# Performance work log

Hardware: AMD Instinct MI355X
Metric: run time of the kernel (lower is better)

The kernel has to match this reference:

```python
import jax, jax.numpy as jnp
import numpy as np

B, T, D, H = 4, 4096, 2048, 128  # batch, seq, n_embd, head_size


def setup_inputs() -> dict:
    key = jax.random.key(0)
    ks = jax.random.split(key, 7)
    s = 1.0 / np.sqrt(D)
    return {
        "x": jax.random.normal(ks[0], (B, T, D), dtype=jnp.float32),
        "Wk": jax.random.normal(ks[1], (D, H), dtype=jnp.float32) * s,
        "bk": jax.random.normal(ks[2], (H,), dtype=jnp.float32) * 0.02,
        "Wq": jax.random.normal(ks[3], (D, H), dtype=jnp.float32) * s,
        "bq": jax.random.normal(ks[4], (H,), dtype=jnp.float32) * 0.02,
        "Wv": jax.random.normal(ks[5], (D, H), dtype=jnp.float32) * s,
        "bv": jax.random.normal(ks[6], (H,), dtype=jnp.float32) * 0.02,
    }


def reference(x, Wk, bk, Wq, bq, Wv, bv):
    # q, k, v projections: [B, T, H]
    q = x @ Wq + bq
    k = x @ Wk + bk
    v = x @ Wv + bv
    scale = jnp.asarray(H, x.dtype) ** -0.5
    # causal attention scores [B, T, T]
    scores = jnp.einsum("bth,bsh->bts", q, k) * scale
    causal = jnp.tril(jnp.ones((T, T), dtype=bool))
    scores = jnp.where(causal, scores, jnp.asarray(-jnp.inf, x.dtype))
    probs = jax.nn.softmax(scores, axis=-1)
    # output [B, T, H]
    return jnp.einsum("bts,bsh->bth", probs, v)
```

## Files before the change

### kernel.cpp

```cpp
#include <hip/hip_runtime.h>

namespace {

typedef float f32x4 __attribute__((ext_vector_type(4)));
typedef short bf16x8 __attribute__((ext_vector_type(8)));

constexpr float SM_SCALE = 0.08838834764831845f;

#define MFMA16(a, b, c) __builtin_amdgcn_mfma_f32_16x16x32_bf16((a), (b), (c), 0, 0, 0)

__device__ __forceinline__ unsigned short bf16_rne(float x) {
  unsigned u = __float_as_uint(x);
  u += 0x7fffu + ((u >> 16) & 1u);
  return (unsigned short)(u >> 16);
}
__device__ __forceinline__ float bf16f(unsigned short h) {
  return __uint_as_float(((unsigned)h) << 16);
}
__device__ __forceinline__ void gld16(const void* g, void* l) {
  __builtin_amdgcn_global_load_lds(
      (const __attribute__((address_space(1))) unsigned int*)g,
      (__attribute__((address_space(3))) unsigned int*)l, 16, 0, 0);
}
__device__ __forceinline__ uint4 pack8(const unsigned short* h) {
  uint4 u;
  u.x = (unsigned)h[0] | ((unsigned)h[1] << 16);
  u.y = (unsigned)h[2] | ((unsigned)h[3] << 16);
  u.z = (unsigned)h[4] | ((unsigned)h[5] << 16);
  u.w = (unsigned)h[6] | ((unsigned)h[7] << 16);
  return u;
}

__global__ void prep_w(const float* __restrict__ Wq, const float* __restrict__ Wk,
                       const float* __restrict__ Wv,
                       unsigned short* __restrict__ WtH, unsigned short* __restrict__ WtL) {
  const int tg = blockIdx.x * 256 + threadIdx.x;
  const int mi = tg >> 15;
  const int rem = tg & 32767;
  const int n = rem & 127;
  const int k0 = (rem >> 7) * 8;
  const float* W = (mi == 0) ? Wq : ((mi == 1) ? Wk : Wv);
  unsigned short hv[8], lv[8];
#pragma unroll
  for (int e = 0; e < 8; ++e) {
    float xx = W[(size_t)(k0 + e) * 128 + n];
    unsigned short hh = bf16_rne(xx);
    hv[e] = hh;
    lv[e] = bf16_rne(xx - bf16f(hh));
  }
  const size_t off = (size_t)mi * 262144 + (size_t)n * 2048 + k0;
  *(uint4*)(WtH + off) = pack8(hv);
  *(uint4*)(WtL + off) = pack8(lv);
}

__global__ __launch_bounds__(256, 2) void qkv_gemm(
    const float* __restrict__ x,
    const unsigned short* __restrict__ WtH, const unsigned short* __restrict__ WtL,
    const float* __restrict__ bq, const float* __restrict__ bk, const float* __restrict__ bv,
    unsigned short* __restrict__ qh, unsigned short* __restrict__ ql,
    unsigned short* __restrict__ kh, unsigned short* __restrict__ kl,
    unsigned short* __restrict__ vTh, unsigned short* __restrict__ vTl) {
  __shared__ __align__(16) unsigned short sm[32768];
  unsigned short* AsH = sm;
  unsigned short* AsL = sm + 8192;
  unsigned short* BsH = sm + 16384;
  unsigned short* BsL = sm + 24576;

  const int mi = blockIdx.x;
  const int m0 = blockIdx.y * 128;
  const int t = threadIdx.x;
  const int w = t >> 6, l = t & 63, g = l >> 4, lm = l & 15;
  const int wr = w >> 1, wc = w & 1;
  const int sw = (lm & 7) << 3;
  const unsigned short* WhP = WtH + (size_t)mi * 262144;
  const unsigned short* WlP = WtL + (size_t)mi * 262144;
  const float* bias = (mi == 0) ? bq : ((mi == 1) ? bk : bv);

  const int arow = t >> 4, ac4 = (t & 15) * 4;
  const int nsub = l >> 3, kk0 = (l & 7) * 8;

  const f32x4 zf = {0.f, 0.f, 0.f, 0.f};
  f32x4 acc[4][4];
#pragma unroll
  for (int m = 0; m < 4; ++m)
#pragma unroll
    for (int n = 0; n < 4; ++n) acc[m][n] = zf;

  float4 av[8];
#pragma unroll
  for (int i = 0; i < 8; ++i)
    av[i] = *(const float4*)(x + (size_t)(m0 + i * 16 + arow) * 2048 + ac4);

  for (int kc = 0; kc < 2048; kc += 64) {
    __syncthreads();
#pragma unroll
    for (int i = 0; i < 4; ++i) {
      const int blk = w * 4 + i;
      const int n = blk * 8 + nsub;
      const size_t go = (size_t)n * 2048 + kc + (kk0 ^ ((n & 7) << 3));
      gld16(WhP + go, BsH + blk * 512);
      gld16(WlP + go, BsL + blk * 512);
    }
#pragma unroll
    for (int i = 0; i < 8; ++i) {
      const int row = i * 16 + arow;
      const int idx = row * 64 + (ac4 ^ ((row & 7) << 3));
      ushort4 hh, ll;
      hh.x = bf16_rne(av[i].x); ll.x = bf16_rne(av[i].x - bf16f(hh.x));
      hh.y = bf16_rne(av[i].y); ll.y = bf16_rne(av[i].y - bf16f(hh.y));
      hh.z = bf16_rne(av[i].z); ll.z = bf16_rne(av[i].z - bf16f(hh.z));
      hh.w = bf16_rne(av[i].w); ll.w = bf16_rne(av[i].w - bf16f(hh.w));
      *(ushort4*)&AsH[idx] = hh;
      *(ushort4*)&AsL[idx] = ll;
    }
    __syncthreads();

    if (kc + 64 < 2048) {
#pragma unroll
      for (int i = 0; i < 8; ++i)
        av[i] = *(const float4*)(x + (size_t)(m0 + i * 16 + arow) * 2048 + kc + 64 + ac4);
    }

    __builtin_amdgcn_s_setprio(1);
#pragma unroll
    for (int ks = 0; ks < 2; ++ks) {
      const int kb = ks * 32 + g * 8;
      bf16x8 ah[4], al_[4], bh_[4], bl_[4];
#pragma unroll
      for (int m = 0; m < 4; ++m) {
        const int row = wr * 64 + m * 16 + lm;
        const int idx = row * 64 + (kb ^ sw);
        ah[m] = *(const bf16x8*)&AsH[idx];
        al_[m] = *(const bf16x8*)&AsL[idx];
      }
#pragma unroll
      for (int n = 0; n < 4; ++n) {
        const int row = wc * 64 + n * 16 + lm;
        const int idx = row * 64 + (kb ^ sw);
        bh_[n] = *(const bf16x8*)&BsH[idx];
        bl_[n] = *(const bf16x8*)&BsL[idx];
      }
#pragma unroll
      for (int m = 0; m < 4; ++m)
#pragma unroll
        for (int n = 0; n < 4; ++n) {
          acc[m][n] = MFMA16(ah[m], bh_[n], acc[m][n]);
          acc[m][n] = MFMA16(ah[m], bl_[n], acc[m][n]);
          acc[m][n] = MFMA16(al_[m], bh_[n], acc[m][n]);
        }
    }
    __builtin_amdgcn_s_setprio(0);
  }

  __syncthreads();
  float* Cb = (float*)sm;
#pragma unroll
  for (int n = 0; n < 4; ++n) {
    const int col = wc * 64 + n * 16 + lm;
    const float bn = bias[col];
#pragma unroll
    for (int m = 0; m < 4; ++m)
#pragma unroll
      for (int r = 0; r < 4; ++r)
        Cb[(wr * 64 + m * 16 + g * 4 + r) * 128 + col] = acc[m][n][r] + bn;
  }
  __syncthreads();

  if (mi < 2) {
    unsigned short* oh = (mi == 0) ? qh : kh;
    unsigned short* ol = (mi == 0) ? ql : kl;
    const int c8 = (t & 15) * 8;
#pragma unroll
    for (int i = 0; i < 8; ++i) {
      const int row = i * 16 + (t >> 4);
      float v8[8];
      *(float4*)(v8)     = *(const float4*)&Cb[row * 128 + c8];
      *(float4*)(v8 + 4) = *(const float4*)&Cb[row * 128 + c8 + 4];
      unsigned short h8[8], l8[8];
#pragma unroll
      for (int j = 0; j < 8; ++j) {
        h8[j] = bf16_rne(v8[j]);
        l8[j] = bf16_rne(v8[j] - bf16f(h8[j]));
      }
      const size_t o = (size_t)(m0 + row) * 128 + c8;
      *(uint4*)(oh + o) = pack8(h8);
      *(uint4*)(ol + o) = pack8(l8);
    }
  } else {
    const int bidx = m0 >> 12, tb0 = m0 & 4095;
    const int tb8 = (t & 15) * 8;
#pragma unroll
    for (int i = 0; i < 8; ++i) {
      const int h = i * 16 + (t >> 4);
      float v8[8];
#pragma unroll
      for (int j = 0; j < 8; ++j) v8[j] = Cb[(tb8 + j) * 128 + h];
      unsigned short h8[8], l8[8];
#pragma unroll
      for (int j = 0; j < 8; ++j) {
        h8[j] = bf16_rne(v8[j]);
        l8[j] = bf16_rne(v8[j] - bf16f(h8[j]));
      }
      const size_t o = ((size_t)bidx * 128 + h) * 4096 + tb0 + tb8;
      *(uint4*)(vTh + o) = pack8(h8);
      *(uint4*)(vTl + o) = pack8(l8);
    }
  }
}

__global__ __launch_bounds__(256, 2) void attn(
    const unsigned short* __restrict__ qh, const unsigned short* __restrict__ ql,
    const unsigned short* __restrict__ kh, const unsigned short* __restrict__ kl,
    const unsigned short* __restrict__ vTh, const unsigned short* __restrict__ vTl,
    float* __restrict__ OP, float* __restrict__ ML) {
  __shared__ __align__(16) unsigned short sm[40960];
  unsigned short* KhL = sm;
  unsigned short* KlL = sm + 8192;
  unsigned short* VhL = sm + 16384;
  unsigned short* VlL = sm + 24576;
  unsigned short* PhL = sm + 32768;
  unsigned short* PlL = sm + 36864;

  const int b = blockIdx.y, bx = blockIdx.x;
  const int pj = bx >> 2, s = bx & 3;
  const int t = threadIdx.x, w = t >> 6, l = t & 63, g = l >> 4, lm = l & 15;
  const int sw8 = (lm & 7) << 3;
  const size_t bT = (size_t)b * 4096;
  const f32x4 zf = {0.f, 0.f, 0.f, 0.f};

  const int krow_l = l >> 4;
  const int kh8 = (l & 15) * 8;
  const int vrow_l = l >> 3;
  const int vk8 = (l & 7) * 8;

  for (int pass = 0; pass < 2; ++pass) {
    const int qb = pass ? (63 - pj) : pj;
    const int q0 = qb * 64;
    const int part = b * 256 + qb * 4 + s;

    bf16x8 qfh[4], qfl[4];
    const size_t qoff = (bT + q0 + w * 16 + lm) * 128;
#pragma unroll
    for (int ks = 0; ks < 4; ++ks) {
      qfh[ks] = *(const bf16x8*)(qh + qoff + ks * 32 + g * 8);
      qfl[ks] = *(const bf16x8*)(ql + qoff + ks * 32 + g * 8);
    }

    f32x4 o[8];
#pragma unroll
    for (int n = 0; n < 8; ++n) o[n] = zf;
    float mrow = -1e30f, lrow = 0.f;
    const int qg = q0 + w * 16 + lm;
    const int nt = qb + 1;

    for (int ti = s; ti < nt; ti += 4) {
      const int t0 = ti * 64;
      __syncthreads();
#pragma unroll
      for (int i = 0; i < 4; ++i) {
        const int j = w * 4 + i;
        const int krow = 4 * j + krow_l;
        const size_t kgo = (bT + t0 + krow) * 128 + (kh8 ^ ((krow & 7) << 3));
        gld16(kh + kgo, KhL + j * 512);
        gld16(kl + kgo, KlL + j * 512);
        const int hrow = 8 * j + vrow_l;
        const size_t vgo = ((size_t)b * 128 + hrow) * 4096 + t0 + (vk8 ^ ((hrow & 7) << 3));
        gld16(vTh + vgo, VhL + j * 512);
        gld16(vTl + vgo, VlL + j * 512);
      }
      __syncthreads();

      f32x4 sa[4] = {zf, zf, zf, zf};
      __builtin_amdgcn_s_setprio(1);
#pragma unroll
      for (int ks = 0; ks < 4; ++ks) {
        const int kb = (ks * 32 + g * 8) ^ sw8;
#pragma unroll
        for (int m = 0; m < 4; ++m) {
          const bf16x8 kf = *(const bf16x8*)&KhL[(m * 16 + lm) * 128 + kb];
          const bf16x8 lf = *(const bf16x8*)&KlL[(m * 16 + lm) * 128 + kb];
          sa[m] = MFMA16(kf, qfh[ks], sa[m]);
          sa[m] = MFMA16(kf, qfl[ks], sa[m]);
          sa[m] = MFMA16(lf, qfh[ks], sa[m]);
        }
      }
      __builtin_amdgcn_s_setprio(0);

      float pv_[16];
      float mt = -1e30f;
#pragma unroll
      for (int m = 0; m < 4; ++m)
#pragma unroll
        for (int r = 0; r < 4; ++r) {
          const int kvg = t0 + m * 16 + g * 4 + r;
          const float sv = (kvg <= qg) ? sa[m][r] * SM_SCALE : -1e30f;
          pv_[m * 4 + r] = sv;
          mt = fmaxf(mt, sv);
        }
      mt = fmaxf(mt, __shfl_xor(mt, 16));
      mt = fmaxf(mt, __shfl_xor(mt, 32));
      const float mnew = fmaxf(mrow, mt);
      const float sc = __expf(mrow - mnew);
      float lsum = 0.f;
#pragma unroll
      for (int j = 0; j < 16; ++j) {
        const float pe = (pv_[j] > -9e29f) ? __expf(pv_[j] - mnew) : 0.f;
        pv_[j] = pe;
        lsum += pe;
      }
      lsum += __shfl_xor(lsum, 16);
      lsum += __shfl_xor(lsum, 32);
      lrow = lrow * sc + lsum;
      mrow = mnew;
      float scr[4];
#pragma unroll
      for (int r = 0; r < 4; ++r) scr[r] = __shfl(sc, g * 4 + r);
#pragma unroll
      for (int n = 0; n < 8; ++n)
#pragma unroll
        for (int r = 0; r < 4; ++r) o[n][r] *= scr[r];

      const int wb = w * 1024;
#pragma unroll
      for (int m = 0; m < 4; ++m)
#pragma unroll
        for (int j2 = 0; j2 < 2; ++j2) {
          const int kv0 = m * 16 + g * 4 + j2 * 2;
          const float p0f = pv_[m * 4 + j2 * 2];
          const float p1f = pv_[m * 4 + j2 * 2 + 1];
          ushort2 h2, l2;
          h2.x = bf16_rne(p0f); l2.x = bf16_rne(p0f - bf16f(h2.x));
          h2.y = bf16_rne(p1f); l2.y = bf16_rne(p1f - bf16f(h2.y));
          *(ushort2*)&PhL[wb + lm * 64 + (kv0 ^ sw8)] = h2;
          *(ushort2*)&PlL[wb + lm * 64 + (kv0 ^ sw8)] = l2;
        }
      const bf16x8 pAh0 = *(const bf16x8*)&PhL[wb + lm * 64 + ((g * 8) ^ sw8)];
      const bf16x8 pAl0 = *(const bf16x8*)&PlL[wb + lm * 64 + ((g * 8) ^ sw8)];
      const bf16x8 pAh1 = *(const bf16x8*)&PhL[wb + lm * 64 + ((32 + g * 8) ^ sw8)];
      const bf16x8 pAl1 = *(const bf16x8*)&PlL[wb + lm * 64 + ((32 + g * 8) ^ sw8)];

      __builtin_amdgcn_s_setprio(1);
#pragma unroll
      for (int n = 0; n < 8; ++n) {
        const int vb = (n * 16 + lm) * 64;
        const bf16x8 vh0 = *(const bf16x8*)&VhL[vb + ((g * 8) ^ sw8)];
        const bf16x8 vl0 = *(const bf16x8*)&VlL[vb + ((g * 8) ^ sw8)];
        o[n] = MFMA16(pAh0, vh0, o[n]);
        o[n] = MFMA16(pAh0, vl0, o[n]);
        o[n] = MFMA16(pAl0, vh0, o[n]);
        const bf16x8 vh1 = *(const bf16x8*)&VhL[vb + ((32 + g * 8) ^ sw8)];
        const bf16x8 vl1 = *(const bf16x8*)&VlL[vb + ((32 + g * 8) ^ sw8)];
        o[n] = MFMA16(pAh1, vh1, o[n]);
        o[n] = MFMA16(pAh1, vl1, o[n]);
        o[n] = MFMA16(pAl1, vh1, o[n]);
      }
      __builtin_amdgcn_s_setprio(0);
    }

    float* OPp = OP + (size_t)part * 8192;
#pragma unroll
    for (int n = 0; n < 8; ++n)
#pragma unroll
      for (int r = 0; r < 4; ++r)
        OPp[(size_t)(w * 16 + g * 4 + r) * 128 + n * 16 + lm] = o[n][r];
    if (l < 16) {
      ML[((size_t)part * 64 + w * 16 + l) * 2 + 0] = mrow;
      ML[((size_t)part * 64 + w * 16 + l) * 2 + 1] = lrow;
    }
  }
}

__global__ void combine(const float* __restrict__ OP, const float* __restrict__ ML,
                        float* __restrict__ out) {
  const int x = blockIdx.x;
  const int b = x >> 6, qb = x & 63;
  const int p0 = b * 256 + qb * 4;
  const int t = threadIdx.x;
  const int r = t >> 2, hq = (t & 3) * 32;
  float m[4], ll[4];
#pragma unroll
  for (int s2 = 0; s2 < 4; ++s2) {
    m[s2]  = ML[((size_t)(p0 + s2) * 64 + r) * 2 + 0];
    ll[s2] = ML[((size_t)(p0 + s2) * 64 + r) * 2 + 1];
  }
  const float mx = fmaxf(fmaxf(m[0], m[1]), fmaxf(m[2], m[3]));
  float wgt[4], den = 0.f;
#pragma unroll
  for (int s2 = 0; s2 < 4; ++s2) {
    wgt[s2] = __expf(m[s2] - mx);
    den += wgt[s2] * ll[s2];
  }
  const float inv = 1.f / den;
  float* op = out + ((size_t)(b * 4096 + qb * 64 + r)) * 128 + hq;
#pragma unroll
  for (int j = 0; j < 8; ++j) {
    float ax = 0.f, ay = 0.f, az = 0.f, aw = 0.f;
#pragma unroll
    for (int s2 = 0; s2 < 4; ++s2) {
      const float4 pv = *(const float4*)(OP + ((size_t)(p0 + s2) * 64 + r) * 128 + hq + j * 4);
      ax += wgt[s2] * pv.x; ay += wgt[s2] * pv.y;
      az += wgt[s2] * pv.z; aw += wgt[s2] * pv.w;
    }
    float4 ov; ov.x = ax * inv; ov.y = ay * inv; ov.z = az * inv; ov.w = aw * inv;
    *(float4*)(op + j * 4) = ov;
  }
}

}

extern "C" void kernel_launch(void* const* d_in, const int* in_sizes, int n_in,
                              void* d_out, int out_size, void* d_ws, size_t ws_size,
                              hipStream_t stream) {
  const float* x  = (const float*)d_in[0];
  const float* Wk = (const float*)d_in[1];
  const float* bk = (const float*)d_in[2];
  const float* Wq = (const float*)d_in[3];
  const float* bq = (const float*)d_in[4];
  const float* Wv = (const float*)d_in[5];
  const float* bv = (const float*)d_in[6];
  float* out = (float*)d_out;

  unsigned short* WtH = (unsigned short*)d_ws;
  unsigned short* WtL = WtH + 786432;
  unsigned short* qh  = WtL + 786432;
  unsigned short* ql  = qh + 2097152;
  unsigned short* kh  = ql + 2097152;
  unsigned short* kl  = kh + 2097152;
  unsigned short* vTh = kl + 2097152;
  unsigned short* vTl = vTh + 2097152;
  float* OP = (float*)(vTl + 2097152);
  float* ML = OP + (size_t)1024 * 8192;

  prep_w<<<384, 256, 0, stream>>>(Wq, Wk, Wv, WtH, WtL);
  qkv_gemm<<<dim3(3, 128), 256, 0, stream>>>(x, WtH, WtL, bq, bk, bv,
                                             qh, ql, kh, kl, vTh, vTl);
  attn<<<dim3(128, 4), 256, 0, stream>>>(qh, ql, kh, kl, vTh, vTl, OP, ML);
  combine<<<256, 256, 0, stream>>>(OP, ML, out);
}
```

Baseline: 380.7 us.

## Retile QKV GEMM with double-buffered weights and 128-row attention blocks

The QKV GEMM now uses 64-row M tiles over a 768-block remapped grid and double-buffers the weight tiles in LDS, so the next K-chunk's loads overlap the current MFMAs. The attention kernel now gives each block 128 query rows (two 16-row tiles per wave) instead of running two 64-row passes, so each K/V tile loaded into LDS is reused across twice as many queries. Partial buffers and the combine kernel are re-indexed to match. The cost is more registers per wave in attention (doubled accumulators and Q fragments), less even causal load balancing, and more LDS in the GEMM.

```diff
diff --git a/kernel.cpp b/kernel.cpp
--- a/kernel.cpp
+++ b/kernel.cpp
@@ -60,14 +60,14 @@
     unsigned short* __restrict__ qh, unsigned short* __restrict__ ql,
     unsigned short* __restrict__ kh, unsigned short* __restrict__ kl,
     unsigned short* __restrict__ vTh, unsigned short* __restrict__ vTl) {
-  __shared__ __align__(16) unsigned short sm[32768];
+  __shared__ __align__(16) unsigned short sm[40960];
   unsigned short* AsH = sm;
-  unsigned short* AsL = sm + 8192;
-  unsigned short* BsH = sm + 16384;
-  unsigned short* BsL = sm + 24576;
-
-  const int mi = blockIdx.x;
-  const int m0 = blockIdx.y * 128;
+  unsigned short* AsL = sm + 4096;
+
+  const int bid = blockIdx.x;
+  const int L = 96 * (bid & 7) + (bid >> 3);
+  const int mi = L % 3;
+  const int m0 = (L / 3) * 64;
   const int t = threadIdx.x;
   const int w = t >> 6, l = t & 63, g = l >> 4, lm = l & 15;
   const int wr = w >> 1, wc = w & 1;
@@ -77,33 +77,34 @@
   const float* bias = (mi == 0) ? bq : ((mi == 1) ? bk : bv);
 
   const int arow = t >> 4, ac4 = (t & 15) * 4;
-  const int nsub = l >> 3, kk0 = (l & 7) * 8;
+  const int brow_l = l >> 3, bk8 = (l & 7) * 8;
 
   const f32x4 zf = {0.f, 0.f, 0.f, 0.f};
-  f32x4 acc[4][4];
-#pragma unroll
-  for (int m = 0; m < 4; ++m)
+  f32x4 acc[2][4];
+#pragma unroll
+  for (int m = 0; m < 2; ++m)
 #pragma unroll
     for (int n = 0; n < 4; ++n) acc[m][n] = zf;
 
-  float4 av[8];
-#pragma unroll
-  for (int i = 0; i < 8; ++i)
-    av[i] = *(const float4*)(x + (size_t)(m0 + i * 16 + arow) * 2048 + ac4);
-
+  float4 av[4];
+#pragma unroll
+  for (int i = 0; i < 4; ++i) {
+    const int j = w * 4 + i;
+    const int n = j * 8 + brow_l;
+    const size_t go = (size_t)n * 2048 + 0 + (bk8 ^ ((n & 7) << 3));
+    gld16(WhP + go, sm + 8192 + j * 512);
+    gld16(WlP + go, sm + 16384 + j * 512);
+  }
+#pragma unroll
+  for (int i = 0; i < 4; ++i)
+    av[i] = *(const float4*)(x + (size_t)(m0 + arow + 16 * i) * 2048 + ac4);
+
+  int cur = 0;
   for (int kc = 0; kc < 2048; kc += 64) {
     __syncthreads();
 #pragma unroll
     for (int i = 0; i < 4; ++i) {
-      const int blk = w * 4 + i;
-      const int n = blk * 8 + nsub;
-      const size_t go = (size_t)n * 2048 + kc + (kk0 ^ ((n & 7) << 3));
-      gld16(WhP + go, BsH + blk * 512);
-      gld16(WlP + go, BsL + blk * 512);
-    }
-#pragma unroll
-    for (int i = 0; i < 8; ++i) {
-      const int row = i * 16 + arow;
+      const int row = arow + 16 * i;
       const int idx = row * 64 + (ac4 ^ ((row & 7) << 3));
       ushort4 hh, ll;
       hh.x = bf16_rne(av[i].x); ll.x = bf16_rne(av[i].x - bf16f(hh.x));
@@ -117,18 +118,28 @@
 
     if (kc + 64 < 2048) {
 #pragma unroll
-      for (int i = 0; i < 8; ++i)
-        av[i] = *(const float4*)(x + (size_t)(m0 + i * 16 + arow) * 2048 + kc + 64 + ac4);
-    }
-
+      for (int i = 0; i < 4; ++i) {
+        const int j = w * 4 + i;
+        const int n = j * 8 + brow_l;
+        const size_t go = (size_t)n * 2048 + (kc + 64) + (bk8 ^ ((n & 7) << 3));
+        gld16(WhP + go, sm + 8192 + (cur ^ 1) * 16384 + j * 512);
+        gld16(WlP + go, sm + 8192 + (cur ^ 1) * 16384 + 8192 + j * 512);
+      }
+#pragma unroll
+      for (int i = 0; i < 4; ++i)
+        av[i] = *(const float4*)(x + (size_t)(m0 + arow + 16 * i) * 2048 + kc + 64 + ac4);
+    }
+
+    const unsigned short* BH = sm + 8192 + cur * 16384;
+    const unsigned short* BL = BH + 8192;
     __builtin_amdgcn_s_setprio(1);
 #pragma unroll
     for (int ks = 0; ks < 2; ++ks) {
       const int kb = ks * 32 + g * 8;
-      bf16x8 ah[4], al_[4], bh_[4], bl_[4];
-#pragma unroll
-      for (int m = 0; m < 4; ++m) {
-        const int row = wr * 64 + m * 16 + lm;
+      bf16x8 ah[2], al_[2], bh_[4], bl_[4];
+#pragma unroll
+      for (int m = 0; m < 2; ++m) {
+        const int row = wr * 32 + m * 16 + lm;
         const int idx = row * 64 + (kb ^ sw);
         ah[m] = *(const bf16x8*)&AsH[idx];
         al_[m] = *(const bf16x8*)&AsL[idx];
@@ -137,11 +148,11 @@
       for (int n = 0; n < 4; ++n) {
         const int row = wc * 64 + n * 16 + lm;
         const int idx = row * 64 + (kb ^ sw);
-        bh_[n] = *(const bf16x8*)&BsH[idx];
-        bl_[n] = *(const bf16x8*)&BsL[idx];
-      }
-#pragma unroll
-      for (int m = 0; m < 4; ++m)
+        bh_[n] = *(const bf16x8*)&BH[idx];
+        bl_[n] = *(const bf16x8*)&BL[idx];
+      }
+#pragma unroll
+      for (int m = 0; m < 2; ++m)
 #pragma unroll
         for (int n = 0; n < 4; ++n) {
           acc[m][n] = MFMA16(ah[m], bh_[n], acc[m][n]);
@@ -150,6 +161,7 @@
         }
     }
     __builtin_amdgcn_s_setprio(0);
+    cur ^= 1;
   }
 
   __syncthreads();
@@ -159,10 +171,10 @@
     const int col = wc * 64 + n * 16 + lm;
     const float bn = bias[col];
 #pragma unroll
-    for (int m = 0; m < 4; ++m)
+    for (int m = 0; m < 2; ++m)
 #pragma unroll
       for (int r = 0; r < 4; ++r)
-        Cb[(wr * 64 + m * 16 + g * 4 + r) * 128 + col] = acc[m][n][r] + bn;
+        Cb[(wr * 32 + m * 16 + g * 4 + r) * 128 + col] = acc[m][n][r] + bn;
   }
   __syncthreads();
 
@@ -171,7 +183,7 @@
     unsigned short* ol = (mi == 0) ? ql : kl;
     const int c8 = (t & 15) * 8;
 #pragma unroll
-    for (int i = 0; i < 8; ++i) {
+    for (int i = 0; i < 4; ++i) {
       const int row = i * 16 + (t >> 4);
       float v8[8];
       *(float4*)(v8)     = *(const float4*)&Cb[row * 128 + c8];
@@ -188,20 +200,20 @@
     }
   } else {
     const int bidx = m0 >> 12, tb0 = m0 & 4095;
-    const int tb8 = (t & 15) * 8;
-#pragma unroll
-    for (int i = 0; i < 8; ++i) {
-      const int h = i * 16 + (t >> 4);
+    const int tc8 = (t & 7) * 8;
+#pragma unroll
+    for (int i = 0; i < 4; ++i) {
+      const int h = i * 32 + (t >> 3);
       float v8[8];
 #pragma unroll
-      for (int j = 0; j < 8; ++j) v8[j] = Cb[(tb8 + j) * 128 + h];
+      for (int j = 0; j < 8; ++j) v8[j] = Cb[(tc8 + j) * 128 + h];
       unsigned short h8[8], l8[8];
 #pragma unroll
       for (int j = 0; j < 8; ++j) {
         h8[j] = bf16_rne(v8[j]);
         l8[j] = bf16_rne(v8[j] - bf16f(h8[j]));
       }
-      const size_t o = ((size_t)bidx * 128 + h) * 4096 + tb0 + tb8;
+      const size_t o = ((size_t)bidx * 128 + h) * 4096 + tb0 + tc8;
       *(uint4*)(vTh + o) = pack8(h8);
       *(uint4*)(vTl + o) = pack8(l8);
     }
@@ -222,7 +234,10 @@
   unsigned short* PlL = sm + 36864;
 
   const int b = blockIdx.y, bx = blockIdx.x;
-  const int pj = bx >> 2, s = bx & 3;
+  const int qb = 31 - (bx >> 2);
+  const int s = bx & 3;
+  const int q0 = qb * 128;
+  const int part = b * 128 + qb * 4 + s;
   const int t = threadIdx.x, w = t >> 6, l = t & 63, g = l >> 4, lm = l & 15;
   const int sw8 = (lm & 7) << 3;
   const size_t bT = (size_t)b * 4096;
@@ -233,59 +248,67 @@
   const int vrow_l = l >> 3;
   const int vk8 = (l & 7) * 8;
 
-  for (int pass = 0; pass < 2; ++pass) {
-    const int qb = pass ? (63 - pj) : pj;
-    const int q0 = qb * 64;
-    const int part = b * 256 + qb * 4 + s;
-
-    bf16x8 qfh[4], qfl[4];
-    const size_t qoff = (bT + q0 + w * 16 + lm) * 128;
+  bf16x8 qfh[2][4], qfl[2][4];
+#pragma unroll
+  for (int qt = 0; qt < 2; ++qt) {
+    const size_t qoff = (bT + q0 + w * 32 + qt * 16 + lm) * 128;
 #pragma unroll
     for (int ks = 0; ks < 4; ++ks) {
-      qfh[ks] = *(const bf16x8*)(qh + qoff + ks * 32 + g * 8);
-      qfl[ks] = *(const bf16x8*)(ql + qoff + ks * 32 + g * 8);
-    }
-
-    f32x4 o[8];
-#pragma unroll
-    for (int n = 0; n < 8; ++n) o[n] = zf;
-    float mrow = -1e30f, lrow = 0.f;
-    const int qg = q0 + w * 16 + lm;
-    const int nt = qb + 1;
-
-    for (int ti = s; ti < nt; ti += 4) {
-      const int t0 = ti * 64;
-      __syncthreads();
-#pragma unroll
-      for (int i = 0; i < 4; ++i) {
-        const int j = w * 4 + i;
-        const int krow = 4 * j + krow_l;
-        const size_t kgo = (bT + t0 + krow) * 128 + (kh8 ^ ((krow & 7) << 3));
-        gld16(kh + kgo, KhL + j * 512);
-        gld16(kl + kgo, KlL + j * 512);
-        const int hrow = 8 * j + vrow_l;
-        const size_t vgo = ((size_t)b * 128 + hrow) * 4096 + t0 + (vk8 ^ ((hrow & 7) << 3));
-        gld16(vTh + vgo, VhL + j * 512);
-        gld16(vTl + vgo, VlL + j * 512);
-      }
-      __syncthreads();
-
-      f32x4 sa[4] = {zf, zf, zf, zf};
-      __builtin_amdgcn_s_setprio(1);
-#pragma unroll
-      for (int ks = 0; ks < 4; ++ks) {
-        const int kb = (ks * 32 + g * 8) ^ sw8;
-#pragma unroll
-        for (int m = 0; m < 4; ++m) {
-          const bf16x8 kf = *(const bf16x8*)&KhL[(m * 16 + lm) * 128 + kb];
-          const bf16x8 lf = *(const bf16x8*)&KlL[(m * 16 + lm) * 128 + kb];
-          sa[m] = MFMA16(kf, qfh[ks], sa[m]);
-          sa[m] = MFMA16(kf, qfl[ks], sa[m]);
-          sa[m] = MFMA16(lf, qfh[ks], sa[m]);
-        }
-      }
-      __builtin_amdgcn_s_setprio(0);
-
+      qfh[qt][ks] = *(const bf16x8*)(qh + qoff + ks * 32 + g * 8);
+      qfl[qt][ks] = *(const bf16x8*)(ql + qoff + ks * 32 + g * 8);
+    }
+  }
+
+  f32x4 o[2][8];
+#pragma unroll
+  for (int qt = 0; qt < 2; ++qt)
+#pragma unroll
+    for (int n = 0; n < 8; ++n) o[qt][n] = zf;
+  float mrow[2] = {-1e30f, -1e30f}, lrow[2] = {0.f, 0.f};
+  const int nt = 2 * qb + 2;
+  const int wb = w * 1024;
+
+  for (int ti = s; ti < nt; ti += 4) {
+    const int t0 = ti * 64;
+    __syncthreads();
+#pragma unroll
+    for (int i = 0; i < 4; ++i) {
+      const int j = w * 4 + i;
+      const int krow = 4 * j + krow_l;
+      const size_t kgo = (bT + t0 + krow) * 128 + (kh8 ^ ((krow & 7) << 3));
+      gld16(kh + kgo, KhL + j * 512);
+      gld16(kl + kgo, KlL + j * 512);
+      const int hrow = 8 * j + vrow_l;
+      const size_t vgo = ((size_t)b * 128 + hrow) * 4096 + t0 + (vk8 ^ ((hrow & 7) << 3));
+      gld16(vTh + vgo, VhL + j * 512);
+      gld16(vTl + vgo, VlL + j * 512);
+    }
+    __syncthreads();
+
+    f32x4 sa[4][2];
+#pragma unroll
+    for (int m = 0; m < 4; ++m) { sa[m][0] = zf; sa[m][1] = zf; }
+    __builtin_amdgcn_s_setprio(1);
+#pragma unroll
+    for (int ks = 0; ks < 4; ++ks) {
+      const int kb = (ks * 32 + g * 8) ^ sw8;
+#pragma unroll
+      for (int m = 0; m < 4; ++m) {
+        const bf16x8 kf = *(const bf16x8*)&KhL[(m * 16 + lm) * 128 + kb];
+        const bf16x8 lf = *(const bf16x8*)&KlL[(m * 16 + lm) * 128 + kb];
+        sa[m][0] = MFMA16(kf, qfh[0][ks], sa[m][0]);
+        sa[m][0] = MFMA16(kf, qfl[0][ks], sa[m][0]);
+        sa[m][0] = MFMA16(lf, qfh[0][ks], sa[m][0]);
+        sa[m][1] = MFMA16(kf, qfh[1][ks], sa[m][1]);
+        sa[m][1] = MFMA16(kf, qfl[1][ks], sa[m][1]);
+        sa[m][1] = MFMA16(lf, qfh[1][ks], sa[m][1]);
+      }
+    }
+    __builtin_amdgcn_s_setprio(0);
+
+#pragma unroll
+    for (int qt = 0; qt < 2; ++qt) {
+      const int qg = q0 + w * 32 + qt * 16 + lm;
       float pv_[16];
       float mt = -1e30f;
 #pragma unroll
@@ -293,14 +316,14 @@
 #pragma unroll
         for (int r = 0; r < 4; ++r) {
           const int kvg = t0 + m * 16 + g * 4 + r;
-          const float sv = (kvg <= qg) ? sa[m][r] * SM_SCALE : -1e30f;
+          const float sv = (kvg <= qg) ? sa[m][qt][r] * SM_SCALE : -1e30f;
           pv_[m * 4 + r] = sv;
           mt = fmaxf(mt, sv);
         }
       mt = fmaxf(mt, __shfl_xor(mt, 16));
       mt = fmaxf(mt, __shfl_xor(mt, 32));
-      const float mnew = fmaxf(mrow, mt);
-      const float sc = __expf(mrow - mnew);
+      const float mnew = fmaxf(mrow[qt], mt);
+      const float sc = __expf(mrow[qt] - mnew);
       float lsum = 0.f;
 #pragma unroll
       for (int j = 0; j < 16; ++j) {
@@ -310,17 +333,16 @@
       }
       lsum += __shfl_xor(lsum, 16);
       lsum += __shfl_xor(lsum, 32);
-      lrow = lrow * sc + lsum;
-      mrow = mnew;
+      lrow[qt] = lrow[qt] * sc + lsum;
+      mrow[qt] = mnew;
       float scr[4];
 #pragma unroll
       for (int r = 0; r < 4; ++r) scr[r] = __shfl(sc, g * 4 + r);
 #pragma unroll
       for (int n = 0; n < 8; ++n)
 #pragma unroll
-        for (int r = 0; r < 4; ++r) o[n][r] *= scr[r];
-
-      const int wb = w * 1024;
+        for (int r = 0; r < 4; ++r) o[qt][n][r] *= scr[r];
+
 #pragma unroll
       for (int m = 0; m < 4; ++m)
 #pragma unroll
@@ -345,43 +367,50 @@
         const int vb = (n * 16 + lm) * 64;
         const bf16x8 vh0 = *(const bf16x8*)&VhL[vb + ((g * 8) ^ sw8)];
         const bf16x8 vl0 = *(const bf16x8*)&VlL[vb + ((g * 8) ^ sw8)];
-        o[n] = MFMA16(pAh0, vh0, o[n]);
-        o[n] = MFMA16(pAh0, vl0, o[n]);
-        o[n] = MFMA16(pAl0, vh0, o[n]);
+        o[qt][n] = MFMA16(pAh0, vh0, o[qt][n]);
+        o[qt][n] = MFMA16(pAh0, vl0, o[qt][n]);
+        o[qt][n] = MFMA16(pAl0, vh0, o[qt][n]);
         const bf16x8 vh1 = *(const bf16x8*)&VhL[vb + ((32 + g * 8) ^ sw8)];
         const bf16x8 vl1 = *(const bf16x8*)&VlL[vb + ((32 + g * 8) ^ sw8)];
-        o[n] = MFMA16(pAh1, vh1, o[n]);
-        o[n] = MFMA16(pAh1, vl1, o[n]);
-        o[n] = MFMA16(pAl1, vh1, o[n]);
+        o[qt][n] = MFMA16(pAh1, vh1, o[qt][n]);
+        o[qt][n] = MFMA16(pAh1, vl1, o[qt][n]);
+        o[qt][n] = MFMA16(pAl1, vh1, o[qt][n]);
       }
       __builtin_amdgcn_s_setprio(0);
     }
-
-    float* OPp = OP + (size_t)part * 8192;
+  }
+
+  float* OPp = OP + (size_t)part * 16384;
+#pragma unroll
+  for (int qt = 0; qt < 2; ++qt)
 #pragma unroll
     for (int n = 0; n < 8; ++n)
 #pragma unroll
       for (int r = 0; r < 4; ++r)
-        OPp[(size_t)(w * 16 + g * 4 + r) * 128 + n * 16 + lm] = o[n][r];
-    if (l < 16) {
-      ML[((size_t)part * 64 + w * 16 + l) * 2 + 0] = mrow;
-      ML[((size_t)part * 64 + w * 16 + l) * 2 + 1] = lrow;
+        OPp[(size_t)(w * 32 + qt * 16 + g * 4 + r) * 128 + n * 16 + lm] = o[qt][n][r];
+  if (l < 16) {
+#pragma unroll
+    for (int qt = 0; qt < 2; ++qt) {
+      ML[((size_t)part * 128 + w * 32 + qt * 16 + l) * 2 + 0] = mrow[qt];
+      ML[((size_t)part * 128 + w * 32 + qt * 16 + l) * 2 + 1] = lrow[qt];
     }
   }
 }
 
 __global__ void combine(const float* __restrict__ OP, const float* __restrict__ ML,
                         float* __restrict__ out) {
-  const int x = blockIdx.x;
-  const int b = x >> 6, qb = x & 63;
-  const int p0 = b * 256 + qb * 4;
+  const int xg = blockIdx.x;
+  const int b = xg >> 6;
   const int t = threadIdx.x;
   const int r = t >> 2, hq = (t & 3) * 32;
+  const int rowb = (xg & 63) * 64 + r;
+  const int qb = rowb >> 7, rl = rowb & 127;
+  const int p0 = b * 128 + qb * 4;
   float m[4], ll[4];
 #pragma unroll
   for (int s2 = 0; s2 < 4; ++s2) {
-    m[s2]  = ML[((size_t)(p0 + s2) * 64 + r) * 2 + 0];
-    ll[s2] = ML[((size_t)(p0 + s2) * 64 + r) * 2 + 1];
+    m[s2]  = ML[((size_t)(p0 + s2) * 128 + rl) * 2 + 0];
+    ll[s2] = ML[((size_t)(p0 + s2) * 128 + rl) * 2 + 1];
   }
   const float mx = fmaxf(fmaxf(m[0], m[1]), fmaxf(m[2], m[3]));
   float wgt[4], den = 0.f;
@@ -391,13 +420,13 @@
     den += wgt[s2] * ll[s2];
   }
   const float inv = 1.f / den;
-  float* op = out + ((size_t)(b * 4096 + qb * 64 + r)) * 128 + hq;
+  float* op = out + ((size_t)(b * 4096 + rowb)) * 128 + hq;
 #pragma unroll
   for (int j = 0; j < 8; ++j) {
     float ax = 0.f, ay = 0.f, az = 0.f, aw = 0.f;
 #pragma unroll
     for (int s2 = 0; s2 < 4; ++s2) {
-      const float4 pv = *(const float4*)(OP + ((size_t)(p0 + s2) * 64 + r) * 128 + hq + j * 4);
+      const float4 pv = *(const float4*)(OP + ((size_t)(p0 + s2) * 16384 + rl * 128 + hq + j * 4));
       ax += wgt[s2] * pv.x; ay += wgt[s2] * pv.y;
       az += wgt[s2] * pv.z; aw += wgt[s2] * pv.w;
     }
@@ -429,11 +458,11 @@
   unsigned short* vTh = kl + 2097152;
   unsigned short* vTl = vTh + 2097152;
   float* OP = (float*)(vTl + 2097152);
-  float* ML = OP + (size_t)1024 * 8192;
+  float* ML = OP + (size_t)512 * 16384;
 
   prep_w<<<384, 256, 0, stream>>>(Wq, Wk, Wv, WtH, WtL);
-  qkv_gemm<<<dim3(3, 128), 256, 0, stream>>>(x, WtH, WtL, bq, bk, bv,
-                                             qh, ql, kh, kl, vTh, vTl);
+  qkv_gemm<<<768, 256, 0, stream>>>(x, WtH, WtL, bq, bk, bv,
+                                    qh, ql, kh, kl, vTh, vTl);
   attn<<<dim3(128, 4), 256, 0, stream>>>(qh, ql, kh, kl, vTh, vTl, OP, ML);
   combine<<<256, 256, 0, stream>>>(OP, ML, out);
 }
```

Result: slower. 411.5 us (+8.1%).
